# Kernel optimization log

Hardware: AMD Instinct MI355X
Metric: run time of the kernel (lower is better)

## Reference

```python
import jax, jax.numpy as jnp
import numpy as np

NQ = 4            # num_qubits
DIM = 2 ** NQ     # 16-dim complex state

def _rx(theta):
    c = jnp.cos(theta / 2.0); s = jnp.sin(theta / 2.0)
    return jnp.array([[c, -1j * s], [-1j * s, c]], dtype=jnp.complex64)

def _ry(theta):
    c = jnp.cos(theta / 2.0); s = jnp.sin(theta / 2.0)
    return jnp.array([[c, -s], [s, c]], dtype=jnp.complex64)

def _apply_1q(state, q, U):
    # state: [B, 16] complex; apply 2x2 unitary U on qubit q (qubit 0 = MSB)
    B = state.shape[0]
    st = state.reshape((B,) + (2,) * NQ)
    st = jnp.moveaxis(st, 1 + q, -1)
    st = st @ U.T
    st = jnp.moveaxis(st, -1, 1 + q)
    return st.reshape(B, DIM)

def _apply_cnot(state, c, t):
    # flip target qubit t where control qubit c == 1
    B = state.shape[0]
    st = state.reshape((B,) + (2,) * NQ)
    st = jnp.moveaxis(st, (1 + c, 1 + t), (-2, -1))
    st = jnp.stack([st[..., 0, :], st[..., 1, ::-1]], axis=-2)
    st = jnp.moveaxis(st, (-2, -1), (1 + c, 1 + t))
    return st.reshape(B, DIM)

def _circuit(state):
    rx1, ry1 = _rx(0.1), _ry(0.2)
    rx2, ry2 = _rx(0.3), _ry(0.4)
    for q in range(NQ):
        state = _apply_1q(state, q, rx1)
        state = _apply_1q(state, q, ry1)
    for q in range(NQ - 1):
        state = _apply_cnot(state, q, q + 1)
    for q in range(NQ):
        state = _apply_1q(state, q, rx2)
        state = _apply_1q(state, q, ry2)
    return state

def setup_inputs() -> dict:
    key = jax.random.key(0)
    ks = jax.random.split(key, 9)
    B = 65536
    return {
        'x':   jax.random.normal(ks[0], (B, 784), dtype=jnp.float32),
        'We1': jax.random.normal(ks[1], (784, 256), dtype=jnp.float32) * 0.05,
        'be1': jnp.zeros((256,), dtype=jnp.float32),
        'We2': jax.random.normal(ks[2], (256, 32), dtype=jnp.float32) * 0.05,
        'be2': jnp.zeros((32,), dtype=jnp.float32),
        'W1':  jax.random.normal(ks[3], (32, 128), dtype=jnp.float32) * 0.05,
        'b1':  jnp.zeros((128,), dtype=jnp.float32),
        'W2':  jax.random.normal(ks[4], (128, 10), dtype=jnp.float32) * 0.05,
        'b2':  jnp.zeros((10,), dtype=jnp.float32),
    }

def reference(x, We1, be1, We2, be2, W1, b1, W2, b2):
    # encoder: Linear(784,256) -> ReLU -> Linear(256,32) -> Tanh
    h = jax.nn.relu(x @ We1 + be1)
    enc = jnp.tanh(h @ We2 + be2)               # [B, 32]
    psi = (enc[:, :DIM] + 1j * enc[:, DIM:]).astype(jnp.complex64)
    norm = jnp.sqrt(jnp.sum(jnp.abs(psi) ** 2, axis=1, keepdims=True))
    psi = psi / norm
    psi = _circuit(psi)                          # [B, 16] complex
    feat = jnp.concatenate([psi.real, psi.imag], axis=1)  # [B, 32]
    # classifier: Linear(32,128) -> ReLU -> (Dropout=identity in eval) -> Linear(128,10)
    out = jax.nn.relu(feat @ W1 + b1) @ W2 + b2
    return out
```

## Files before the change

kernel.cpp:

```cpp
#include <hip/hip_runtime.h>
#include <stdint.h>

#define DEVINL __device__ __forceinline__

typedef short bf16x8 __attribute__((ext_vector_type(8)));
typedef float f32x4  __attribute__((ext_vector_type(4)));

DEVINL uint16_t f2bf(float f) {
    uint32_t u = __builtin_bit_cast(uint32_t, f);
    uint32_t r = u + 0x7fffu + ((u >> 16) & 1u);
    return (uint16_t)(r >> 16);
}

DEVINL f32x4 mfma16x16x32(bf16x8 a, bf16x8 b, f32x4 c) {
    return __builtin_amdgcn_mfma_f32_16x16x32_bf16(a, b, c, 0, 0, 0);
}

DEVINL void lds_barrier() {
    asm volatile("s_waitcnt lgkmcnt(0)\n\ts_barrier" ::: "memory");
}

#define WS_WE1T 0
#define WS_WE2T 409600
#define WS_W1T  425984
#define WS_W2T  434176

__global__ __launch_bounds__(256) void prep_weights(
    const float* __restrict__ We1, const float* __restrict__ We2,
    const float* __restrict__ W1,  const float* __restrict__ W2,
    uint16_t* __restrict__ We1T, uint16_t* __restrict__ We2T,
    uint16_t* __restrict__ W1T,  uint16_t* __restrict__ W2T) {
    int tid = blockIdx.x * 256 + threadIdx.x;
    if (tid < 256 * 800) {
        int n = tid / 800, k = tid % 800;
        We1T[tid] = (k < 784) ? f2bf(We1[k * 256 + n]) : (uint16_t)0;
        return;
    }
    int t2 = tid - 256 * 800;
    if (t2 < 32 * 256) {
        int n = t2 / 256, k = t2 % 256;
        We2T[t2] = f2bf(We2[k * 32 + n]);
        return;
    }
    int t3 = t2 - 32 * 256;
    if (t3 < 128 * 32) {
        int n = t3 / 32, k = t3 % 32;
        W1T[t3] = f2bf(W1[k * 128 + n]);
        return;
    }
    int t4 = t3 - 128 * 32;
    if (t4 < 16 * 128) {
        int n = t4 / 128, k = t4 % 128;
        W2T[t4] = (n < 10) ? f2bf(W2[k * 10 + n]) : (uint16_t)0;
        return;
    }
}

DEVINL void apply_rx(float* sr, float* si, int bit, float c, float s) {
    #pragma unroll
    for (int i = 0; i < 16; i++) {
        if (!(i & bit)) {
            int j = i | bit;
            float r0 = sr[i], i0 = si[i], r1 = sr[j], i1 = si[j];
            sr[i] = c * r0 + s * i1;  si[i] = c * i0 - s * r1;
            sr[j] = c * r1 + s * i0;  si[j] = c * i1 - s * r0;
        }
    }
}
DEVINL void apply_ry(float* sr, float* si, int bit, float c, float s) {
    #pragma unroll
    for (int i = 0; i < 16; i++) {
        if (!(i & bit)) {
            int j = i | bit;
            float r0 = sr[i], i0 = si[i], r1 = sr[j], i1 = si[j];
            sr[i] = c * r0 - s * r1;  si[i] = c * i0 - s * i1;
            sr[j] = s * r0 + c * r1;  si[j] = s * i0 + c * i1;
        }
    }
}
DEVINL void apply_cnot(float* sr, float* si, int cb, int tb) {
    #pragma unroll
    for (int i = 0; i < 16; i++) {
        if ((i & cb) && !(i & tb)) {
            int j = i | tb;
            float tr = sr[i]; sr[i] = sr[j]; sr[j] = tr;
            float ti = si[i]; si[i] = si[j]; si[j] = ti;
        }
    }
}
DEVINL void circuit(float* sr, float* si) {
    const float C1 = 0.99875026039496628f, S1 = 0.04997916927067833f;
    const float C2 = 0.99500416527802582f, S2 = 0.09983341664682815f;
    const float C3 = 0.98877107793604227f, S3 = 0.14943813247359922f;
    const float C4 = 0.98006657784124163f, S4 = 0.19866933079506122f;
    #pragma unroll
    for (int q = 0; q < 4; q++) {
        int bit = 8 >> q;
        apply_rx(sr, si, bit, C1, S1);
        apply_ry(sr, si, bit, C2, S2);
    }
    apply_cnot(sr, si, 8, 4);
    apply_cnot(sr, si, 4, 2);
    apply_cnot(sr, si, 2, 1);
    #pragma unroll
    for (int q = 0; q < 4; q++) {
        int bit = 8 >> q;
        apply_rx(sr, si, bit, C3, S3);
        apply_ry(sr, si, bit, C4, S4);
    }
}

__global__ __launch_bounds__(256, 4) void fused_kernel(
    const float* __restrict__ x, const uint16_t* __restrict__ We1T,
    const float* __restrict__ be1,
    const uint16_t* __restrict__ We2T, const float* __restrict__ be2,
    const uint16_t* __restrict__ W1T, const float* __restrict__ b1,
    const uint16_t* __restrict__ W2T, const float* __restrict__ b2,
    float* __restrict__ out) {
    __shared__ __align__(16) char smem[34816];
    uint16_t* Als = (uint16_t*)smem;
    uint16_t* Htile = (uint16_t*)smem;
    float*    encls  = (float*)smem;
    uint16_t* featls = (uint16_t*)(smem + 8448);
    uint16_t* a1ls   = (uint16_t*)(smem + 13568);

    const int t = threadIdx.x;
    const int rowbase = blockIdx.x * 64;
    const int w  = t >> 6;
    const int l  = t & 63;
    const int lm = l & 15;
    const int lq = l >> 4;

    f32x4 acc[4][4] = {};

    const int ar = t >> 2;
    const int aq = t & 3;
    const float* xrow = x + (size_t)(rowbase + ar) * 784;

    const uint16_t* bbase = We1T + (size_t)(w * 64 + lm) * 800 + lq * 8;

    {
        float4 v0 = *(const float4*)(xrow + aq * 8);
        float4 v1 = *(const float4*)(xrow + aq * 8 + 4);
        union { uint4 u4; uint16_t us[8]; } pk;
        pk.us[0] = f2bf(v0.x); pk.us[1] = f2bf(v0.y);
        pk.us[2] = f2bf(v0.z); pk.us[3] = f2bf(v0.w);
        pk.us[4] = f2bf(v1.x); pk.us[5] = f2bf(v1.y);
        pk.us[6] = f2bf(v1.z); pk.us[7] = f2bf(v1.w);
        *(uint4*)&Als[8 * t] = pk.u4;
    }
    float4 va0 = *(const float4*)(xrow + 32 + aq * 8);
    float4 va1 = *(const float4*)(xrow + 32 + aq * 8 + 4);
    lds_barrier();

    int buf = 0;
    for (int k0 = 0; k0 < 800; k0 += 32) {
        const uint16_t* AlsCur = Als + buf * 2048;
        bf16x8 afr[4];
        #pragma unroll
        for (int mi = 0; mi < 4; mi++)
            afr[mi] = *(const bf16x8*)&AlsCur[(mi * 16 + lm) * 32 + lq * 8];

        bf16x8 bfr[4];
        #pragma unroll
        for (int ni = 0; ni < 4; ni++)
            bfr[ni] = *(const bf16x8*)(bbase + (size_t)(ni * 16) * 800 + k0);

        if (k0 + 32 < 800) {
            union { uint4 u4; uint16_t us[8]; } pk;
            pk.us[0] = f2bf(va0.x); pk.us[1] = f2bf(va0.y);
            pk.us[2] = f2bf(va0.z); pk.us[3] = f2bf(va0.w);
            pk.us[4] = f2bf(va1.x); pk.us[5] = f2bf(va1.y);
            pk.us[6] = f2bf(va1.z); pk.us[7] = f2bf(va1.w);
            *(uint4*)&Als[(buf ^ 1) * 2048 + 8 * t] = pk.u4;
            int kn = k0 + 64;
            if (kn < 800) {
                int c = kn + aq * 8;
                if (c < 784) {
                    va0 = *(const float4*)(xrow + c);
                    va1 = *(const float4*)(xrow + c + 4);
                } else {
                    va0 = make_float4(0.f, 0.f, 0.f, 0.f);
                    va1 = make_float4(0.f, 0.f, 0.f, 0.f);
                }
            }
        }

        #pragma unroll
        for (int mi = 0; mi < 4; mi++)
            #pragma unroll
            for (int ni = 0; ni < 4; ni++)
                acc[mi][ni] = mfma16x16x32(afr[mi], bfr[ni], acc[mi][ni]);

        lds_barrier();
        buf ^= 1;
    }

    #pragma unroll
    for (int ni = 0; ni < 4; ni++) {
        int n = w * 64 + ni * 16 + lm;
        float bias = be1[n];
        #pragma unroll
        for (int mi = 0; mi < 4; mi++) {
            #pragma unroll
            for (int i = 0; i < 4; i++) {
                int r = mi * 16 + lq * 4 + i;
                float v = acc[mi][ni][i] + bias;
                v = v > 0.f ? v : 0.f;
                Htile[r * 272 + n] = f2bf(v);
            }
        }
    }
    __syncthreads();

    f32x4 acc2[2] = {};
    #pragma unroll
    for (int k0 = 0; k0 < 256; k0 += 32) {
        bf16x8 af = *(const bf16x8*)&Htile[(w * 16 + lm) * 272 + k0 + lq * 8];
        #pragma unroll
        for (int ni = 0; ni < 2; ni++) {
            bf16x8 bf = *(const bf16x8*)&We2T[(ni * 16 + lm) * 256 + k0 + lq * 8];
            acc2[ni] = mfma16x16x32(af, bf, acc2[ni]);
        }
    }
    __syncthreads();

    #pragma unroll
    for (int ni = 0; ni < 2; ni++) {
        int col = ni * 16 + lm;
        float bias = be2[col];
        #pragma unroll
        for (int i = 0; i < 4; i++) {
            int r = w * 16 + lq * 4 + i;
            encls[r * 33 + col] = tanhf(acc2[ni][i] + bias);
        }
    }
    __syncthreads();

    if (t < 64) {
        float e[32];
        #pragma unroll
        for (int j = 0; j < 32; j++) e[j] = encls[t * 33 + j];
        float s = 0.f;
        #pragma unroll
        for (int j = 0; j < 32; j++) s += e[j] * e[j];
        float inv = 1.0f / sqrtf(s);
        float sr[16], si[16];
        #pragma unroll
        for (int i = 0; i < 16; i++) { sr[i] = e[i] * inv; si[i] = e[16 + i] * inv; }
        circuit(sr, si);
        #pragma unroll
        for (int i = 0; i < 16; i++) {
            featls[t * 40 + i]      = f2bf(sr[i]);
            featls[t * 40 + 16 + i] = f2bf(si[i]);
        }
    }
    __syncthreads();

    f32x4 acc3[8] = {};
    {
        bf16x8 af = *(const bf16x8*)&featls[(w * 16 + lm) * 40 + lq * 8];
        #pragma unroll
        for (int ni = 0; ni < 8; ni++) {
            bf16x8 bf = *(const bf16x8*)&W1T[(ni * 16 + lm) * 32 + lq * 8];
            acc3[ni] = mfma16x16x32(af, bf, acc3[ni]);
        }
    }
    #pragma unroll
    for (int ni = 0; ni < 8; ni++) {
        int col = ni * 16 + lm;
        float bias = b1[col];
        #pragma unroll
        for (int i = 0; i < 4; i++) {
            int r = w * 16 + lq * 4 + i;
            float v = acc3[ni][i] + bias;
            v = v > 0.f ? v : 0.f;
            a1ls[r * 136 + col] = f2bf(v);
        }
    }

    f32x4 acc4 = {};
    #pragma unroll
    for (int k0 = 0; k0 < 128; k0 += 32) {
        bf16x8 af = *(const bf16x8*)&a1ls[(w * 16 + lm) * 136 + k0 + lq * 8];
        bf16x8 bf = *(const bf16x8*)&W2T[lm * 128 + k0 + lq * 8];
        acc4 = mfma16x16x32(af, bf, acc4);
    }
    if (lm < 10) {
        float bias = b2[lm];
        #pragma unroll
        for (int i = 0; i < 4; i++) {
            int r = rowbase + w * 16 + lq * 4 + i;
            out[(size_t)r * 10 + lm] = acc4[i] + bias;
        }
    }
}

extern "C" void kernel_launch(void* const* d_in, const int* in_sizes, int n_in,
                              void* d_out, int out_size, void* d_ws, size_t ws_size,
                              hipStream_t stream) {
    const float* x   = (const float*)d_in[0];
    const float* We1 = (const float*)d_in[1];
    const float* be1 = (const float*)d_in[2];
    const float* We2 = (const float*)d_in[3];
    const float* be2 = (const float*)d_in[4];
    const float* W1  = (const float*)d_in[5];
    const float* b1  = (const float*)d_in[6];
    const float* W2  = (const float*)d_in[7];
    const float* b2  = (const float*)d_in[8];
    float* out = (float*)d_out;

    char* ws = (char*)d_ws;
    uint16_t* We1T = (uint16_t*)(ws + WS_WE1T);
    uint16_t* We2T = (uint16_t*)(ws + WS_WE2T);
    uint16_t* W1T  = (uint16_t*)(ws + WS_W1T);
    uint16_t* W2T  = (uint16_t*)(ws + WS_W2T);

    hipLaunchKernelGGL(prep_weights, dim3(856), dim3(256), 0, stream,
                       We1, We2, W1, W2, We1T, We2T, W1T, W2T);
    hipLaunchKernelGGL(fused_kernel, dim3(1024), dim3(256), 0, stream,
                       x, We1T, be1, We2T, be2, W1T, b1, W2T, b2, out);
}
```

Measured before the change: 337.3 us.

## Load x fragments directly into registers and halve rows per block

The first GEMM no longer stages x through a double-buffered LDS tile with barriers. Each lane loads its fp32 A-fragment straight from global memory, prefetched one k-step ahead, and packs it to bf16 in registers. Rows per block drop from 64 to 32, so the grid doubles, LDS shrinks, and the occupancy hint rises to 5. The later small GEMMs are re-split across the four waves to fit the smaller tile. The trade-off is that all four waves now load the same x rows redundantly instead of sharing one LDS copy. Each We1 fragment is also reused across only 2 M-tiles instead of 4, which doubles weight traffic per row.

```diff
diff --git a/kernel.cpp b/kernel.cpp
--- a/kernel.cpp
+++ b/kernel.cpp
@@ -16,8 +16,13 @@
     return __builtin_amdgcn_mfma_f32_16x16x32_bf16(a, b, c, 0, 0, 0);
 }
 
-DEVINL void lds_barrier() {
-    asm volatile("s_waitcnt lgkmcnt(0)\n\ts_barrier" ::: "memory");
+DEVINL bf16x8 pack8(float4 v0, float4 v1) {
+    union { bf16x8 v; uint16_t us[8]; } pk;
+    pk.us[0] = f2bf(v0.x); pk.us[1] = f2bf(v0.y);
+    pk.us[2] = f2bf(v0.z); pk.us[3] = f2bf(v0.w);
+    pk.us[4] = f2bf(v1.x); pk.us[5] = f2bf(v1.y);
+    pk.us[6] = f2bf(v1.z); pk.us[7] = f2bf(v1.w);
+    return pk.v;
 }
 
 #define WS_WE1T 0
@@ -110,90 +115,69 @@
     }
 }
 
-__global__ __launch_bounds__(256, 4) void fused_kernel(
+__global__ __launch_bounds__(256, 5) void fused_kernel(
     const float* __restrict__ x, const uint16_t* __restrict__ We1T,
     const float* __restrict__ be1,
     const uint16_t* __restrict__ We2T, const float* __restrict__ be2,
     const uint16_t* __restrict__ W1T, const float* __restrict__ b1,
     const uint16_t* __restrict__ W2T, const float* __restrict__ b2,
     float* __restrict__ out) {
-    __shared__ __align__(16) char smem[34816];
-    uint16_t* Als = (uint16_t*)smem;
-    uint16_t* Htile = (uint16_t*)smem;
+    __shared__ __align__(16) char smem[17408];
+    uint16_t* Htile  = (uint16_t*)smem;
     float*    encls  = (float*)smem;
-    uint16_t* featls = (uint16_t*)(smem + 8448);
-    uint16_t* a1ls   = (uint16_t*)(smem + 13568);
+    uint16_t* featls = (uint16_t*)(smem + 4224);
+    uint16_t* a1ls   = (uint16_t*)(smem + 6784);
 
     const int t = threadIdx.x;
-    const int rowbase = blockIdx.x * 64;
+    const int rowbase = blockIdx.x * 32;
     const int w  = t >> 6;
     const int l  = t & 63;
     const int lm = l & 15;
     const int lq = l >> 4;
 
-    f32x4 acc[4][4] = {};
-
-    const int ar = t >> 2;
-    const int aq = t & 3;
-    const float* xrow = x + (size_t)(rowbase + ar) * 784;
-
+    f32x4 acc[2][4] = {};
+
+    const float* arow0 = x + (size_t)(rowbase + lm) * 784 + lq * 8;
+    const float* arow1 = arow0 + 16 * 784;
     const uint16_t* bbase = We1T + (size_t)(w * 64 + lm) * 800 + lq * 8;
 
-    {
-        float4 v0 = *(const float4*)(xrow + aq * 8);
-        float4 v1 = *(const float4*)(xrow + aq * 8 + 4);
-        union { uint4 u4; uint16_t us[8]; } pk;
-        pk.us[0] = f2bf(v0.x); pk.us[1] = f2bf(v0.y);
-        pk.us[2] = f2bf(v0.z); pk.us[3] = f2bf(v0.w);
-        pk.us[4] = f2bf(v1.x); pk.us[5] = f2bf(v1.y);
-        pk.us[6] = f2bf(v1.z); pk.us[7] = f2bf(v1.w);
-        *(uint4*)&Als[8 * t] = pk.u4;
-    }
-    float4 va0 = *(const float4*)(xrow + 32 + aq * 8);
-    float4 va1 = *(const float4*)(xrow + 32 + aq * 8 + 4);
-    lds_barrier();
-
-    int buf = 0;
+    float4 a00 = *(const float4*)(arow0);
+    float4 a01 = *(const float4*)(arow0 + 4);
+    float4 a10 = *(const float4*)(arow1);
+    float4 a11 = *(const float4*)(arow1 + 4);
+
     for (int k0 = 0; k0 < 800; k0 += 32) {
-        const uint16_t* AlsCur = Als + buf * 2048;
-        bf16x8 afr[4];
-        #pragma unroll
-        for (int mi = 0; mi < 4; mi++)
-            afr[mi] = *(const bf16x8*)&AlsCur[(mi * 16 + lm) * 32 + lq * 8];
+        float4 n00, n01, n10, n11;
+        int kn = k0 + 32;
+        if (kn < 800) {
+            int c = kn + lq * 8;
+            if (c < 784) {
+                n00 = *(const float4*)(arow0 + kn);
+                n01 = *(const float4*)(arow0 + kn + 4);
+                n10 = *(const float4*)(arow1 + kn);
+                n11 = *(const float4*)(arow1 + kn + 4);
+            } else {
+                n00 = n01 = n10 = n11 = make_float4(0.f, 0.f, 0.f, 0.f);
+            }
+        } else {
+            n00 = n01 = n10 = n11 = make_float4(0.f, 0.f, 0.f, 0.f);
+        }
 
         bf16x8 bfr[4];
         #pragma unroll
         for (int ni = 0; ni < 4; ni++)
             bfr[ni] = *(const bf16x8*)(bbase + (size_t)(ni * 16) * 800 + k0);
 
-        if (k0 + 32 < 800) {
-            union { uint4 u4; uint16_t us[8]; } pk;
-            pk.us[0] = f2bf(va0.x); pk.us[1] = f2bf(va0.y);
-            pk.us[2] = f2bf(va0.z); pk.us[3] = f2bf(va0.w);
-            pk.us[4] = f2bf(va1.x); pk.us[5] = f2bf(va1.y);
-            pk.us[6] = f2bf(va1.z); pk.us[7] = f2bf(va1.w);
-            *(uint4*)&Als[(buf ^ 1) * 2048 + 8 * t] = pk.u4;
-            int kn = k0 + 64;
-            if (kn < 800) {
-                int c = kn + aq * 8;
-                if (c < 784) {
-                    va0 = *(const float4*)(xrow + c);
-                    va1 = *(const float4*)(xrow + c + 4);
-                } else {
-                    va0 = make_float4(0.f, 0.f, 0.f, 0.f);
-                    va1 = make_float4(0.f, 0.f, 0.f, 0.f);
-                }
-            }
-        }
-
-        #pragma unroll
-        for (int mi = 0; mi < 4; mi++)
-            #pragma unroll
-            for (int ni = 0; ni < 4; ni++)
-                acc[mi][ni] = mfma16x16x32(afr[mi], bfr[ni], acc[mi][ni]);
-
-        lds_barrier();
-        buf ^= 1;
+        bf16x8 afr0 = pack8(a00, a01);
+        bf16x8 afr1 = pack8(a10, a11);
+
+        #pragma unroll
+        for (int ni = 0; ni < 4; ni++) {
+            acc[0][ni] = mfma16x16x32(afr0, bfr[ni], acc[0][ni]);
+            acc[1][ni] = mfma16x16x32(afr1, bfr[ni], acc[1][ni]);
+        }
+
+        a00 = n00; a01 = n01; a10 = n10; a11 = n11;
     }
 
     #pragma unroll
@@ -201,7 +185,7 @@
         int n = w * 64 + ni * 16 + lm;
         float bias = be1[n];
         #pragma unroll
-        for (int mi = 0; mi < 4; mi++) {
+        for (int mi = 0; mi < 2; mi++) {
             #pragma unroll
             for (int i = 0; i < 4; i++) {
                 int r = mi * 16 + lq * 4 + i;
@@ -213,31 +197,29 @@
     }
     __syncthreads();
 
-    f32x4 acc2[2] = {};
+    const int mrow = (w & 1) * 16;
+    const int ncol = (w >> 1) * 16;
+    f32x4 acc2 = {};
     #pragma unroll
     for (int k0 = 0; k0 < 256; k0 += 32) {
-        bf16x8 af = *(const bf16x8*)&Htile[(w * 16 + lm) * 272 + k0 + lq * 8];
-        #pragma unroll
-        for (int ni = 0; ni < 2; ni++) {
-            bf16x8 bf = *(const bf16x8*)&We2T[(ni * 16 + lm) * 256 + k0 + lq * 8];
-            acc2[ni] = mfma16x16x32(af, bf, acc2[ni]);
-        }
-    }
-    __syncthreads();
-
-    #pragma unroll
-    for (int ni = 0; ni < 2; ni++) {
-        int col = ni * 16 + lm;
+        bf16x8 af = *(const bf16x8*)&Htile[(mrow + lm) * 272 + k0 + lq * 8];
+        bf16x8 bf = *(const bf16x8*)&We2T[(ncol + lm) * 256 + k0 + lq * 8];
+        acc2 = mfma16x16x32(af, bf, acc2);
+    }
+    __syncthreads();
+
+    {
+        int col = ncol + lm;
         float bias = be2[col];
         #pragma unroll
         for (int i = 0; i < 4; i++) {
-            int r = w * 16 + lq * 4 + i;
-            encls[r * 33 + col] = tanhf(acc2[ni][i] + bias);
-        }
-    }
-    __syncthreads();
-
-    if (t < 64) {
+            int r = mrow + lq * 4 + i;
+            encls[r * 33 + col] = tanhf(acc2[i] + bias);
+        }
+    }
+    __syncthreads();
+
+    if (t < 32) {
         float e[32];
         #pragma unroll
         for (int j = 0; j < 32; j++) e[j] = encls[t * 33 + j];
@@ -257,41 +239,45 @@
     }
     __syncthreads();
 
-    f32x4 acc3[8] = {};
+    const int nc64 = (w >> 1) * 64;
+    f32x4 acc3[4] = {};
     {
-        bf16x8 af = *(const bf16x8*)&featls[(w * 16 + lm) * 40 + lq * 8];
-        #pragma unroll
-        for (int ni = 0; ni < 8; ni++) {
-            bf16x8 bf = *(const bf16x8*)&W1T[(ni * 16 + lm) * 32 + lq * 8];
+        bf16x8 af = *(const bf16x8*)&featls[(mrow + lm) * 40 + lq * 8];
+        #pragma unroll
+        for (int ni = 0; ni < 4; ni++) {
+            bf16x8 bf = *(const bf16x8*)&W1T[(nc64 + ni * 16 + lm) * 32 + lq * 8];
             acc3[ni] = mfma16x16x32(af, bf, acc3[ni]);
         }
     }
     #pragma unroll
-    for (int ni = 0; ni < 8; ni++) {
-        int col = ni * 16 + lm;
+    for (int ni = 0; ni < 4; ni++) {
+        int col = nc64 + ni * 16 + lm;
         float bias = b1[col];
         #pragma unroll
         for (int i = 0; i < 4; i++) {
-            int r = w * 16 + lq * 4 + i;
+            int r = mrow + lq * 4 + i;
             float v = acc3[ni][i] + bias;
             v = v > 0.f ? v : 0.f;
             a1ls[r * 136 + col] = f2bf(v);
         }
     }
-
-    f32x4 acc4 = {};
-    #pragma unroll
-    for (int k0 = 0; k0 < 128; k0 += 32) {
-        bf16x8 af = *(const bf16x8*)&a1ls[(w * 16 + lm) * 136 + k0 + lq * 8];
-        bf16x8 bf = *(const bf16x8*)&W2T[lm * 128 + k0 + lq * 8];
-        acc4 = mfma16x16x32(af, bf, acc4);
-    }
-    if (lm < 10) {
-        float bias = b2[lm];
-        #pragma unroll
-        for (int i = 0; i < 4; i++) {
-            int r = rowbase + w * 16 + lq * 4 + i;
-            out[(size_t)r * 10 + lm] = acc4[i] + bias;
+    __syncthreads();
+
+    if (w < 2) {
+        f32x4 acc4 = {};
+        #pragma unroll
+        for (int k0 = 0; k0 < 128; k0 += 32) {
+            bf16x8 af = *(const bf16x8*)&a1ls[(w * 16 + lm) * 136 + k0 + lq * 8];
+            bf16x8 bf = *(const bf16x8*)&W2T[lm * 128 + k0 + lq * 8];
+            acc4 = mfma16x16x32(af, bf, acc4);
+        }
+        if (lm < 10) {
+            float bias = b2[lm];
+            #pragma unroll
+            for (int i = 0; i < 4; i++) {
+                int r = rowbase + w * 16 + lq * 4 + i;
+                out[(size_t)r * 10 + lm] = acc4[i] + bias;
+            }
         }
     }
 }
@@ -318,6 +304,6 @@
 
     hipLaunchKernelGGL(prep_weights, dim3(856), dim3(256), 0, stream,
                        We1, We2, W1, W2, We1T, We2T, W1T, W2T);
-    hipLaunchKernelGGL(fused_kernel, dim3(1024), dim3(256), 0, stream,
+    hipLaunchKernelGGL(fused_kernel, dim3(2048), dim3(256), 0, stream,
                        x, We1T, be1, We2T, be2, W1T, b1, W2T, b2, out);
 }
```

Result: slower. 414.3 us (+22.8%).
